# Kernel optimization log

Measured on AMD Instinct MI355X. Metric: run time of the kernel, lower is better.

## Reference

```python
import jax, jax.numpy as jnp
import numpy as np

NUM_HEADS = 16


def setup_inputs() -> dict:
    key = jax.random.key(0)
    ks = jax.random.split(key, 8)
    B, S, H = 2, 2048, 1024
    sd = 1.0 / np.sqrt(H)
    return {
        "x": jax.random.normal(ks[0], (B, S, H), dtype=jnp.float32),
        "mask": jax.random.randint(ks[1], (B, S), 0, 2, dtype=jnp.int32),
        "wq": jax.random.normal(ks[2], (H, H), dtype=jnp.float32) * sd,
        "bq": jnp.zeros((H,), jnp.float32),
        "wk": jax.random.normal(ks[3], (H, H), dtype=jnp.float32) * sd,
        "bk": jnp.zeros((H,), jnp.float32),
        "wv": jax.random.normal(ks[4], (H, H), dtype=jnp.float32) * sd,
        "bv": jnp.zeros((H,), jnp.float32),
        "wo": jax.random.normal(ks[5], (H, H), dtype=jnp.float32) * sd,
        "bo": jnp.zeros((H,), jnp.float32),
        "wg": jax.random.normal(ks[6], (H, H), dtype=jnp.float32) * sd,
        "bg": jnp.zeros((H,), jnp.float32),
    }


def reference(x, mask, wq, bq, wk, bk, wv, bv, wo, bo, wg, bg):
    B, S, H = x.shape
    nh = NUM_HEADS
    hd = H // nh
    scale = hd ** -0.5

    def split_heads(t):  # [B,S,H] -> [B,nh,S,hd]
        return t.reshape(B, S, nh, hd).transpose(0, 2, 1, 3)

    q = split_heads(x @ wq.T + bq)
    k = split_heads(x @ wk.T + bk)
    v = split_heads(x @ wv.T + bv)

    scores = jnp.einsum("bhqd,bhkd->bhqk", q, k) * scale
    # key-padding mask broadcast to [B,1,1,S]
    scores = jnp.where(mask[:, None, None, :] == 0, jnp.float32(-10000.0), scores)
    attn_weights = jax.nn.softmax(scores, axis=-1)  # dropout is identity in eval

    context = jnp.einsum("bhqk,bhkd->bhqd", attn_weights, v)
    context = context.transpose(0, 2, 1, 3).reshape(B, S, H)

    gate_values = jax.nn.sigmoid(context @ wg.T + bg)
    output = (context @ wo.T + bo) * gate_values
    return output, attn_weights
```

## Files before the change

### kernel.cpp

```cpp
#include <hip/hip_runtime.h>
#include <math.h>

#define BB 2
#define SS 2048
#define HH 1024
#define NH 16
#define HD 64
#define LDK 40

typedef __attribute__((ext_vector_type(8))) short short8;
typedef __attribute__((ext_vector_type(4))) float floatx4;

__device__ __forceinline__ unsigned short f2bf(float f) {
    unsigned u = __float_as_uint(f);
    u += 0x7FFF + ((u >> 16) & 1);
    return (unsigned short)(u >> 16);
}
__device__ __forceinline__ float bf2f(unsigned short h) {
    return __uint_as_float((unsigned)h << 16);
}
__device__ __forceinline__ short8 mkshort8(unsigned d0, unsigned d1, unsigned d2, unsigned d3) {
    union { unsigned u[4]; short8 s; } t;
    t.u[0] = d0; t.u[1] = d1; t.u[2] = d2; t.u[3] = d3;
    return t.s;
}

struct SplitJob { const float* src; unsigned short* dh; unsigned short* dl; int n; };
struct SplitJobs { SplitJob j[6]; };

__global__ __launch_bounds__(256) void presplit(SplitJobs jobs)
{
    SplitJob jb = jobs.j[blockIdx.y];
    const int i = (blockIdx.x * 256 + threadIdx.x) * 8;
    if (i >= jb.n) return;
    float4 v0 = *(const float4*)(jb.src + i);
    float4 v1 = *(const float4*)(jb.src + i + 4);
    float f[8] = {v0.x, v0.y, v0.z, v0.w, v1.x, v1.y, v1.z, v1.w};
    union { unsigned short s[8]; uint4 v; } h, l;
#pragma unroll
    for (int j = 0; j < 8; ++j) {
        const unsigned short hs = f2bf(f[j]);
        h.s[j] = hs;
        l.s[j] = f2bf(f[j] - bf2f(hs));
    }
    *(uint4*)(jb.dh + i) = h.v;
    *(uint4*)(jb.dl + i) = l.v;
}

__global__ __launch_bounds__(256) void vtranspose_bf(
    const unsigned short* __restrict__ Vh, const unsigned short* __restrict__ Vl,
    unsigned short* __restrict__ VTh, unsigned short* __restrict__ VTl)
{
    __shared__ __attribute__((aligned(16))) unsigned short t[64][72];
    const int zz = blockIdx.z;
    const int b = zz >> 1;
    const unsigned short* V = (zz & 1) ? Vl : Vh;
    unsigned short* VT = (zz & 1) ? VTl : VTh;
    const int k0 = blockIdx.x * 64;
    const int h = blockIdx.y;
    const int tid = threadIdx.x;
    {
        const int row = tid >> 2, c0 = (tid & 3) * 16;
        const int sw = ((row >> 4) & 3) << 4;
        const unsigned short* g = V + (size_t)(b * SS + k0 + row) * (3 * HH) + h * HD + c0;
        uint4 u0 = *(const uint4*)g;
        uint4 u1 = *(const uint4*)(g + 8);
        *(uint4*)&t[row][c0 ^ sw] = u0;
        *(uint4*)&t[row][(c0 ^ sw) + 8] = u1;
    }
    __syncthreads();
    {
        const int d = tid >> 2, kq = tid & 3;
        const int cs = d ^ (kq << 4);
        union { unsigned short s[16]; uint4 v[2]; } o;
#pragma unroll
        for (int i = 0; i < 16; ++i) o.s[i] = t[kq * 16 + i][cs];
        unsigned short* p = VT + ((size_t)(b * NH + h) * HD + d) * SS + k0 + kq * 16;
        *(uint4*)p = o.v[0];
        *(uint4*)(p + 8) = o.v[1];
    }
}

__global__ __launch_bounds__(256) void attn_fused(
    const unsigned short* __restrict__ QKVh, const unsigned short* __restrict__ QKVl,
    const unsigned short* __restrict__ VTh, const unsigned short* __restrict__ VTl,
    const int* __restrict__ mask,
    float* __restrict__ attn,
    unsigned short* __restrict__ CTXh, unsigned short* __restrict__ CTXl)
{
    __shared__ __attribute__((aligned(16))) unsigned int PS[64 * 64];
    __shared__ float sums[2][64];

    const int tid = threadIdx.x;
    const int wave = tid >> 6, lane = tid & 63;
    const int wm = wave >> 1, wn = wave & 1;
    const int r16 = lane & 15, quad = lane >> 4;

    const int m0 = blockIdx.x * 64;
    const int z  = blockIdx.y;
    const int bz = z >> 4, hz = z & 15;

    short8 fqh[2][2], fql[2][2];
#pragma unroll
    for (int mt = 0; mt < 2; ++mt)
#pragma unroll
        for (int ks = 0; ks < 2; ++ks) {
            const size_t off = (size_t)(bz * SS + m0 + wm * 32 + mt * 16 + r16) * (3 * HH)
                             + hz * HD + ks * 32 + quad * 8;
            fqh[mt][ks] = *(const short8*)(QKVh + off);
            fql[mt][ks] = *(const short8*)(QKVl + off);
        }

    float rsum[2][4];
#pragma unroll
    for (int mt = 0; mt < 2; ++mt)
#pragma unroll
        for (int r = 0; r < 4; ++r) rsum[mt][r] = 0.f;

    for (int nb = 0; nb < 32; ++nb) {
        const int kv0 = nb * 64;
        short8 fkh[2][2], fkl[2][2];
        int mv[2];
#pragma unroll
        for (int nt = 0; nt < 2; ++nt) {
            const int kvr = kv0 + wn * 32 + nt * 16 + r16;
            mv[nt] = mask[bz * SS + kvr];
#pragma unroll
            for (int ks = 0; ks < 2; ++ks) {
                const size_t off = (size_t)(bz * SS + kvr) * (3 * HH) + HH + hz * HD
                                 + ks * 32 + quad * 8;
                fkh[nt][ks] = *(const short8*)(QKVh + off);
                fkl[nt][ks] = *(const short8*)(QKVl + off);
            }
        }
        floatx4 p[2][2];
#pragma unroll
        for (int mt = 0; mt < 2; ++mt)
#pragma unroll
            for (int nt = 0; nt < 2; ++nt) p[mt][nt] = (floatx4){0.f, 0.f, 0.f, 0.f};
#pragma unroll
        for (int mt = 0; mt < 2; ++mt)
#pragma unroll
            for (int nt = 0; nt < 2; ++nt)
#pragma unroll
                for (int ks = 0; ks < 2; ++ks) {
                    p[mt][nt] = __builtin_amdgcn_mfma_f32_16x16x32_bf16(fqh[mt][ks], fkh[nt][ks], p[mt][nt], 0, 0, 0);
                    p[mt][nt] = __builtin_amdgcn_mfma_f32_16x16x32_bf16(fqh[mt][ks], fkl[nt][ks], p[mt][nt], 0, 0, 0);
                    p[mt][nt] = __builtin_amdgcn_mfma_f32_16x16x32_bf16(fql[mt][ks], fkh[nt][ks], p[mt][nt], 0, 0, 0);
                }
#pragma unroll
        for (int mt = 0; mt < 2; ++mt)
#pragma unroll
            for (int nt = 0; nt < 2; ++nt)
#pragma unroll
                for (int r = 0; r < 4; ++r) {
                    const float e = mv[nt] ? __expf(p[mt][nt][r] * 0.125f) : 0.f;
                    rsum[mt][r] += e;
                }
    }
#pragma unroll
    for (int mt = 0; mt < 2; ++mt)
#pragma unroll
        for (int r = 0; r < 4; ++r) {
            float sv = rsum[mt][r];
            sv += __shfl_xor(sv, 1); sv += __shfl_xor(sv, 2);
            sv += __shfl_xor(sv, 4); sv += __shfl_xor(sv, 8);
            if (r16 == 0) sums[wn][wm * 32 + mt * 16 + quad * 4 + r] = sv;
        }
    __syncthreads();
    float inv[2][4];
#pragma unroll
    for (int mt = 0; mt < 2; ++mt)
#pragma unroll
        for (int r = 0; r < 4; ++r) {
            const int row = wm * 32 + mt * 16 + quad * 4 + r;
            inv[mt][r] = 1.0f / (sums[0][row] + sums[1][row]);
        }

    floatx4 accc[2][2];
#pragma unroll
    for (int mt = 0; mt < 2; ++mt)
#pragma unroll
        for (int nt = 0; nt < 2; ++nt) accc[mt][nt] = (floatx4){0.f, 0.f, 0.f, 0.f};

    for (int nb = 0; nb < 32; ++nb) {
        const int kv0 = nb * 64;
        short8 fvh[2][2], fvl[2][2];
#pragma unroll
        for (int nt = 0; nt < 2; ++nt)
#pragma unroll
            for (int kk = 0; kk < 2; ++kk) {
                const size_t off = ((size_t)z * HD + wn * 32 + nt * 16 + r16) * SS
                                 + kv0 + kk * 32 + quad * 8;
                fvh[nt][kk] = *(const short8*)(VTh + off);
                fvl[nt][kk] = *(const short8*)(VTl + off);
            }
        short8 fkh[2][2], fkl[2][2];
        int mv[2];
#pragma unroll
        for (int nt = 0; nt < 2; ++nt) {
            const int kvr = kv0 + wn * 32 + nt * 16 + r16;
            mv[nt] = mask[bz * SS + kvr];
#pragma unroll
            for (int ks = 0; ks < 2; ++ks) {
                const size_t off = (size_t)(bz * SS + kvr) * (3 * HH) + HH + hz * HD
                                 + ks * 32 + quad * 8;
                fkh[nt][ks] = *(const short8*)(QKVh + off);
                fkl[nt][ks] = *(const short8*)(QKVl + off);
            }
        }
        floatx4 p[2][2];
#pragma unroll
        for (int mt = 0; mt < 2; ++mt)
#pragma unroll
            for (int nt = 0; nt < 2; ++nt) p[mt][nt] = (floatx4){0.f, 0.f, 0.f, 0.f};
#pragma unroll
        for (int mt = 0; mt < 2; ++mt)
#pragma unroll
            for (int nt = 0; nt < 2; ++nt)
#pragma unroll
                for (int ks = 0; ks < 2; ++ks) {
                    p[mt][nt] = __builtin_amdgcn_mfma_f32_16x16x32_bf16(fqh[mt][ks], fkh[nt][ks], p[mt][nt], 0, 0, 0);
                    p[mt][nt] = __builtin_amdgcn_mfma_f32_16x16x32_bf16(fqh[mt][ks], fkl[nt][ks], p[mt][nt], 0, 0, 0);
                    p[mt][nt] = __builtin_amdgcn_mfma_f32_16x16x32_bf16(fql[mt][ks], fkh[nt][ks], p[mt][nt], 0, 0, 0);
                }
        __syncthreads();
#pragma unroll
        for (int nt = 0; nt < 2; ++nt) {
            const int kvc = wn * 32 + nt * 16 + r16;
#pragma unroll
            for (int mt = 0; mt < 2; ++mt) {
                const int qb = wm * 32 + mt * 16 + quad * 4;
#pragma unroll
                for (int r = 0; r < 4; ++r) {
                    const float e = mv[nt] ? __expf(p[mt][nt][r] * 0.125f) : 0.f;
                    const float pn = e * inv[mt][r];
                    attn[((size_t)z * SS + m0 + qb + r) * SS + kv0 + kvc] = pn;
                    const unsigned short hv = f2bf(pn);
                    const unsigned short lv = f2bf(pn - bf2f(hv));
                    const int qrow = qb + r;
                    PS[qrow * 64 + (kvc ^ ((qrow & 7) << 2))] =
                        (unsigned)hv | ((unsigned)lv << 16);
                }
            }
        }
        __syncthreads();
#pragma unroll
        for (int mt = 0; mt < 2; ++mt) {
            const int q = wm * 32 + mt * 16 + r16;
            const int sw = (q & 7) << 2;
#pragma unroll
            for (int kk = 0; kk < 2; ++kk) {
                const int kvb = kk * 32 + quad * 8;
                const uint4 a = *(const uint4*)&PS[q * 64 + (kvb ^ sw)];
                const uint4 b = *(const uint4*)&PS[q * 64 + ((kvb + 4) ^ sw)];
                const short8 pah = mkshort8((a.x & 0xffffu) | (a.y << 16),
                                            (a.z & 0xffffu) | (a.w << 16),
                                            (b.x & 0xffffu) | (b.y << 16),
                                            (b.z & 0xffffu) | (b.w << 16));
                const short8 pal = mkshort8((a.x >> 16) | (a.y & 0xffff0000u),
                                            (a.z >> 16) | (a.w & 0xffff0000u),
                                            (b.x >> 16) | (b.y & 0xffff0000u),
                                            (b.z >> 16) | (b.w & 0xffff0000u));
#pragma unroll
                for (int nt = 0; nt < 2; ++nt) {
                    accc[mt][nt] = __builtin_amdgcn_mfma_f32_16x16x32_bf16(pah, fvh[nt][kk], accc[mt][nt], 0, 0, 0);
                    accc[mt][nt] = __builtin_amdgcn_mfma_f32_16x16x32_bf16(pah, fvl[nt][kk], accc[mt][nt], 0, 0, 0);
                    accc[mt][nt] = __builtin_amdgcn_mfma_f32_16x16x32_bf16(pal, fvh[nt][kk], accc[mt][nt], 0, 0, 0);
                }
            }
        }
    }
#pragma unroll
    for (int nt = 0; nt < 2; ++nt) {
        const int dcol = hz * HD + wn * 32 + nt * 16 + r16;
#pragma unroll
        for (int mt = 0; mt < 2; ++mt) {
            const int tok = bz * SS + m0 + wm * 32 + mt * 16 + quad * 4;
#pragma unroll
            for (int r = 0; r < 4; ++r) {
                const float vv = accc[mt][nt][r];
                const unsigned short hv = f2bf(vv);
                const size_t idx = (size_t)(tok + r) * HH + dcol;
                CTXh[idx] = hv;
                CTXl[idx] = f2bf(vv - bf2f(hv));
            }
        }
    }
}

template<int BN, int MODE>
__global__ __launch_bounds__(256) void gemm_bf(
    const unsigned short* __restrict__ Ah, const unsigned short* __restrict__ Al,
    const unsigned short* __restrict__ Bh, const unsigned short* __restrict__ Bl,
    const unsigned short* __restrict__ B2h, const unsigned short* __restrict__ B2l,
    const float* __restrict__ bias, const float* __restrict__ bias2, const float* __restrict__ bias3,
    float* __restrict__ Cf, unsigned short* __restrict__ Ch, unsigned short* __restrict__ Cl,
    int K, int lda, int ldb, int ldc)
{
    constexpr int BM = 128;
    constexpr int MT = 4;
    constexpr int NT = BN / 32;
    constexpr int NSET = (MODE == 3) ? 2 : 1;

    __shared__ __attribute__((aligned(16))) unsigned short AhS[BM * LDK];
    __shared__ __attribute__((aligned(16))) unsigned short AlS[BM * LDK];
    __shared__ __attribute__((aligned(16))) unsigned short BhS[NSET * BN * LDK];
    __shared__ __attribute__((aligned(16))) unsigned short BlS[NSET * BN * LDK];

    const int tid  = threadIdx.x;
    const int lane = tid & 63;
    const int wave = tid >> 6;
    const int wm = wave >> 1, wn = wave & 1;
    const int r16 = lane & 15, quad = lane >> 4;

    const int m0 = blockIdx.y * BM;
    const int n0 = blockIdx.x * BN;

    floatx4 acc[MT][NT][NSET];
#pragma unroll
    for (int mt = 0; mt < MT; ++mt)
#pragma unroll
        for (int nt = 0; nt < NT; ++nt)
#pragma unroll
            for (int s = 0; s < NSET; ++s)
                acc[mt][nt][s] = (floatx4){0.f, 0.f, 0.f, 0.f};

    const int arow = tid >> 1, ac = (tid & 1) * 16;
    const int brow = (BN == 128) ? (tid >> 1) : (tid >> 2);
    const int bc   = (BN == 128) ? ((tid & 1) * 16) : ((tid & 3) * 8);

    const unsigned short* aph = Ah + (size_t)(m0 + arow) * lda + ac;
    const unsigned short* apl = Al + (size_t)(m0 + arow) * lda + ac;
    const unsigned short* bph = Bh + (size_t)(n0 + brow) * ldb + bc;
    const unsigned short* bpl = Bl + (size_t)(n0 + brow) * ldb + bc;
    const unsigned short* b2ph = nullptr;
    const unsigned short* b2pl = nullptr;
    if constexpr (MODE == 3) {
        b2ph = B2h + (size_t)(n0 + brow) * ldb + bc;
        b2pl = B2l + (size_t)(n0 + brow) * ldb + bc;
    }

    for (int kb = 0; kb < K; kb += 32) {
        uint4 avh0 = *(const uint4*)(aph + kb);
        uint4 avh1 = *(const uint4*)(aph + kb + 8);
        uint4 avl0 = *(const uint4*)(apl + kb);
        uint4 avl1 = *(const uint4*)(apl + kb + 8);
        uint4 bvh0 = *(const uint4*)(bph + kb);
        uint4 bvl0 = *(const uint4*)(bpl + kb);
        uint4 bvh1, bvl1, cvh0, cvl0;
        if constexpr (BN == 128) {
            bvh1 = *(const uint4*)(bph + kb + 8);
            bvl1 = *(const uint4*)(bpl + kb + 8);
        }
        if constexpr (MODE == 3) {
            cvh0 = *(const uint4*)(b2ph + kb);
            cvl0 = *(const uint4*)(b2pl + kb);
        }
        __syncthreads();
        *(uint4*)&AhS[arow * LDK + ac]     = avh0;
        *(uint4*)&AhS[arow * LDK + ac + 8] = avh1;
        *(uint4*)&AlS[arow * LDK + ac]     = avl0;
        *(uint4*)&AlS[arow * LDK + ac + 8] = avl1;
        *(uint4*)&BhS[brow * LDK + bc] = bvh0;
        *(uint4*)&BlS[brow * LDK + bc] = bvl0;
        if constexpr (BN == 128) {
            *(uint4*)&BhS[brow * LDK + bc + 8] = bvh1;
            *(uint4*)&BlS[brow * LDK + bc + 8] = bvl1;
        }
        if constexpr (MODE == 3) {
            *(uint4*)&BhS[BN * LDK + brow * LDK + bc] = cvh0;
            *(uint4*)&BlS[BN * LDK + brow * LDK + bc] = cvl0;
        }
        __syncthreads();

        short8 fah[MT], fal[MT], fbh[NSET][NT], fbl[NSET][NT];
#pragma unroll
        for (int mt = 0; mt < MT; ++mt) {
            const int rr = (wm * 64 + mt * 16 + r16) * LDK + quad * 8;
            fah[mt] = *(const short8*)&AhS[rr];
            fal[mt] = *(const short8*)&AlS[rr];
        }
#pragma unroll
        for (int s = 0; s < NSET; ++s)
#pragma unroll
            for (int nt = 0; nt < NT; ++nt) {
                const int rr = s * BN * LDK + (wn * (BN / 2) + nt * 16 + r16) * LDK + quad * 8;
                fbh[s][nt] = *(const short8*)&BhS[rr];
                fbl[s][nt] = *(const short8*)&BlS[rr];
            }
#pragma unroll
        for (int mt = 0; mt < MT; ++mt)
#pragma unroll
            for (int nt = 0; nt < NT; ++nt)
#pragma unroll
                for (int s = 0; s < NSET; ++s) {
                    acc[mt][nt][s] = __builtin_amdgcn_mfma_f32_16x16x32_bf16(fah[mt], fbh[s][nt], acc[mt][nt][s], 0, 0, 0);
                    acc[mt][nt][s] = __builtin_amdgcn_mfma_f32_16x16x32_bf16(fah[mt], fbl[s][nt], acc[mt][nt][s], 0, 0, 0);
                    acc[mt][nt][s] = __builtin_amdgcn_mfma_f32_16x16x32_bf16(fal[mt], fbh[s][nt], acc[mt][nt][s], 0, 0, 0);
                }
    }

    if constexpr (MODE == 0) {
#pragma unroll
        for (int nt = 0; nt < NT; ++nt) {
            const int col = n0 + wn * (BN / 2) + nt * 16 + r16;
            const int seg = col >> 10;
            const float* bp = (seg == 0) ? bias : ((seg == 1) ? bias2 : bias3);
            const float bval = bp[col & (HH - 1)];
#pragma unroll
            for (int mt = 0; mt < MT; ++mt) {
                const int rowb = m0 + wm * 64 + mt * 16 + quad * 4;
#pragma unroll
                for (int r = 0; r < 4; ++r) {
                    const float v = acc[mt][nt][0][r] + bval;
                    const unsigned short hv = f2bf(v);
                    const size_t idx = (size_t)(rowb + r) * ldc + col;
                    Ch[idx] = hv;
                    Cl[idx] = f2bf(v - bf2f(hv));
                }
            }
        }
    }
    if constexpr (MODE == 3) {
#pragma unroll
        for (int nt = 0; nt < NT; ++nt) {
            const int col = n0 + wn * (BN / 2) + nt * 16 + r16;
            const float bov = bias[col], bgv = bias2[col];
#pragma unroll
            for (int mt = 0; mt < MT; ++mt) {
                const int rowb = m0 + wm * 64 + mt * 16 + quad * 4;
#pragma unroll
                for (int r = 0; r < 4; ++r) {
                    const float o = acc[mt][nt][0][r] + bov;
                    const float g = acc[mt][nt][1][r] + bgv;
                    Cf[(size_t)(rowb + r) * ldc + col] = o / (1.f + __expf(-g));
                }
            }
        }
    }
}

extern "C" void kernel_launch(void* const* d_in, const int* in_sizes, int n_in,
                              void* d_out, int out_size, void* d_ws, size_t ws_size,
                              hipStream_t stream)
{
    const float* x    = (const float*)d_in[0];
    const int*   mask = (const int*)d_in[1];
    const float* wq = (const float*)d_in[2];  const float* bq = (const float*)d_in[3];
    const float* wk = (const float*)d_in[4];  const float* bk = (const float*)d_in[5];
    const float* wv = (const float*)d_in[6];  const float* bv = (const float*)d_in[7];
    const float* wo = (const float*)d_in[8];  const float* bo = (const float*)d_in[9];
    const float* wg = (const float*)d_in[10]; const float* bg = (const float*)d_in[11];

    const int M = BB * SS;
    const size_t NTOK = (size_t)M * HH;
    const size_t W1   = (size_t)HH * HH;
    const size_t QKVE = (size_t)M * 3 * HH;

    float* out_main = (float*)d_out;
    float* attn     = (float*)d_out + NTOK;

    unsigned short* p = (unsigned short*)d_ws;
    unsigned short* xh   = p;  p += NTOK;
    unsigned short* xl   = p;  p += NTOK;
    unsigned short* Wqh  = p;  p += 3 * W1;
    unsigned short* Wql  = p;  p += 3 * W1;
    unsigned short* Wgh  = p;  p += 2 * W1;
    unsigned short* Wgl  = p;  p += 2 * W1;
    unsigned short* QKVh = p;  p += QKVE;
    unsigned short* QKVl = p;  p += QKVE;
    unsigned short* VTh  = p;  p += NTOK;
    unsigned short* VTl  = p;  p += NTOK;

    unsigned short* CTXh = xh;
    unsigned short* CTXl = xl;

    SplitJobs jobs;
    jobs.j[0] = SplitJob{x,  xh,           xl,           (int)NTOK};
    jobs.j[1] = SplitJob{wq, Wqh,          Wql,          (int)W1};
    jobs.j[2] = SplitJob{wk, Wqh + W1,     Wql + W1,     (int)W1};
    jobs.j[3] = SplitJob{wv, Wqh + 2 * W1, Wql + 2 * W1, (int)W1};
    jobs.j[4] = SplitJob{wo, Wgh,          Wgl,          (int)W1};
    jobs.j[5] = SplitJob{wg, Wgh + W1,     Wgl + W1,     (int)W1};
    presplit<<<dim3(2048, 6, 1), 256, 0, stream>>>(jobs);

    gemm_bf<128, 0><<<dim3(24, 32, 1), 256, 0, stream>>>(
        xh, xl, Wqh, Wql, nullptr, nullptr,
        bq, bk, bv,
        nullptr, QKVh, QKVl,
        HH, HH, HH, 3 * HH);

    vtranspose_bf<<<dim3(SS / 64, NH, 2 * BB), 256, 0, stream>>>(
        QKVh + 2 * HH, QKVl + 2 * HH, VTh, VTl);

    attn_fused<<<dim3(SS / 64, BB * NH, 1), 256, 0, stream>>>(
        QKVh, QKVl, VTh, VTl, mask, attn, CTXh, CTXl);

    gemm_bf<64, 3><<<dim3(16, 32, 1), 256, 0, stream>>>(
        CTXh, CTXl, Wgh, Wgl, Wgh + W1, Wgl + W1,
        bo, bg, nullptr,
        out_main, nullptr, nullptr,
        HH, HH, HH, HH);

    (void)in_sizes; (void)n_in; (void)out_size; (void)ws_size;
}
```

Baseline: 1.104 ms.

## Stage K tiles into LDS via async global_load_lds and swizzle block-to-XCD mapping

Attention now loads each 64-row K tile (hi and lo bf16 planes) cooperatively into double-buffered, XOR-swizzled shared memory using global_load_lds. The next tile is prefetched while the current one is computed. Previously every wave read K fragments straight from global memory, each wave fetching overlapping data. Block indices in both the attention and GEMM kernels are remapped so that workgroups sharing the same head or tiles land on the same XCD, aiming for better L2 reuse. This adds 32KB of LDS and extra barriers per iteration, which may lower occupancy.

```diff
diff --git a/kernel.cpp b/kernel.cpp
--- a/kernel.cpp
+++ b/kernel.cpp
@@ -10,6 +10,9 @@
 
 typedef __attribute__((ext_vector_type(8))) short short8;
 typedef __attribute__((ext_vector_type(4))) float floatx4;
+
+typedef const __attribute__((address_space(1))) unsigned int* gas1_t;
+typedef __attribute__((address_space(3))) unsigned int* las3_t;
 
 __device__ __forceinline__ unsigned short f2bf(float f) {
     unsigned u = __float_as_uint(f);
@@ -81,6 +84,23 @@
     }
 }
 
+__device__ __forceinline__ void stage_k(
+    unsigned short* KS, const unsigned short* QKVh, const unsigned short* QKVl,
+    int buf, int bz, int hz, int kv0, int tid)
+{
+#pragma unroll
+    for (int i = 0; i < 2; ++i) {
+        const int cid = i * 256 + tid;
+        const int row = cid >> 3;
+        const int cs  = (cid & 7) ^ (row & 7);
+        const size_t goff = (size_t)(bz * SS + kv0 + row) * (3 * HH) + HH + hz * HD + cs * 8;
+        __builtin_amdgcn_global_load_lds((gas1_t)(const void*)(QKVh + goff),
+            (las3_t)(void*)(KS + (buf * 2 + 0) * 4096 + cid * 8), 16, 0, 0);
+        __builtin_amdgcn_global_load_lds((gas1_t)(const void*)(QKVl + goff),
+            (las3_t)(void*)(KS + (buf * 2 + 1) * 4096 + cid * 8), 16, 0, 0);
+    }
+}
+
 __global__ __launch_bounds__(256) void attn_fused(
     const unsigned short* __restrict__ QKVh, const unsigned short* __restrict__ QKVl,
     const unsigned short* __restrict__ VTh, const unsigned short* __restrict__ VTl,
@@ -89,6 +109,7 @@
     unsigned short* __restrict__ CTXh, unsigned short* __restrict__ CTXl)
 {
     __shared__ __attribute__((aligned(16))) unsigned int PS[64 * 64];
+    __shared__ __attribute__((aligned(16))) unsigned short KS[4 * 4096];
     __shared__ float sums[2][64];
 
     const int tid = threadIdx.x;
@@ -96,8 +117,10 @@
     const int wm = wave >> 1, wn = wave & 1;
     const int r16 = lane & 15, quad = lane >> 4;
 
-    const int m0 = blockIdx.x * 64;
-    const int z  = blockIdx.y;
+    const int lin = blockIdx.y * 32 + blockIdx.x;
+    const int swz = (lin & 7) * 128 + (lin >> 3);
+    const int m0 = (swz & 31) * 64;
+    const int z  = swz >> 5;
     const int bz = z >> 4, hz = z & 15;
 
     short8 fqh[2][2], fql[2][2];
@@ -111,26 +134,34 @@
             fql[mt][ks] = *(const short8*)(QKVl + off);
         }
 
+    stage_k(KS, QKVh, QKVl, 0, bz, hz, 0, tid);
+    __syncthreads();
+
     float rsum[2][4];
 #pragma unroll
     for (int mt = 0; mt < 2; ++mt)
 #pragma unroll
         for (int r = 0; r < 4; ++r) rsum[mt][r] = 0.f;
 
+    int cur = 0;
     for (int nb = 0; nb < 32; ++nb) {
         const int kv0 = nb * 64;
+        const int nxt = (nb + 1 < 32) ? (nb + 1) * 64 : 0;
+        stage_k(KS, QKVh, QKVl, cur ^ 1, bz, hz, nxt, tid);
+        int mv[2];
+#pragma unroll
+        for (int nt = 0; nt < 2; ++nt)
+            mv[nt] = mask[bz * SS + kv0 + wn * 32 + nt * 16 + r16];
         short8 fkh[2][2], fkl[2][2];
-        int mv[2];
 #pragma unroll
         for (int nt = 0; nt < 2; ++nt) {
-            const int kvr = kv0 + wn * 32 + nt * 16 + r16;
-            mv[nt] = mask[bz * SS + kvr];
+            const int row = wn * 32 + nt * 16 + r16;
+            const int sx = row & 7;
 #pragma unroll
             for (int ks = 0; ks < 2; ++ks) {
-                const size_t off = (size_t)(bz * SS + kvr) * (3 * HH) + HH + hz * HD
-                                 + ks * 32 + quad * 8;
-                fkh[nt][ks] = *(const short8*)(QKVh + off);
-                fkl[nt][ks] = *(const short8*)(QKVl + off);
+                const int off = row * 64 + ((ks * 4 + quad) ^ sx) * 8;
+                fkh[nt][ks] = *(const short8*)&KS[(cur * 2 + 0) * 4096 + off];
+                fkl[nt][ks] = *(const short8*)&KS[(cur * 2 + 1) * 4096 + off];
             }
         }
         floatx4 p[2][2];
@@ -157,6 +188,8 @@
                     const float e = mv[nt] ? __expf(p[mt][nt][r] * 0.125f) : 0.f;
                     rsum[mt][r] += e;
                 }
+        __syncthreads();
+        cur ^= 1;
     }
 #pragma unroll
     for (int mt = 0; mt < 2; ++mt)
@@ -185,6 +218,7 @@
 
     for (int nb = 0; nb < 32; ++nb) {
         const int kv0 = nb * 64;
+        if (nb + 1 < 32) stage_k(KS, QKVh, QKVl, cur ^ 1, bz, hz, (nb + 1) * 64, tid);
         short8 fvh[2][2], fvl[2][2];
 #pragma unroll
         for (int nt = 0; nt < 2; ++nt)
@@ -195,18 +229,20 @@
                 fvh[nt][kk] = *(const short8*)(VTh + off);
                 fvl[nt][kk] = *(const short8*)(VTl + off);
             }
+        int mv[2];
+#pragma unroll
+        for (int nt = 0; nt < 2; ++nt)
+            mv[nt] = mask[bz * SS + kv0 + wn * 32 + nt * 16 + r16];
         short8 fkh[2][2], fkl[2][2];
-        int mv[2];
 #pragma unroll
         for (int nt = 0; nt < 2; ++nt) {
-            const int kvr = kv0 + wn * 32 + nt * 16 + r16;
-            mv[nt] = mask[bz * SS + kvr];
+            const int row = wn * 32 + nt * 16 + r16;
+            const int sx = row & 7;
 #pragma unroll
             for (int ks = 0; ks < 2; ++ks) {
-                const size_t off = (size_t)(bz * SS + kvr) * (3 * HH) + HH + hz * HD
-                                 + ks * 32 + quad * 8;
-                fkh[nt][ks] = *(const short8*)(QKVh + off);
-                fkl[nt][ks] = *(const short8*)(QKVl + off);
+                const int off = row * 64 + ((ks * 4 + quad) ^ sx) * 8;
+                fkh[nt][ks] = *(const short8*)&KS[(cur * 2 + 0) * 4096 + off];
+                fkl[nt][ks] = *(const short8*)&KS[(cur * 2 + 1) * 4096 + off];
             }
         }
         floatx4 p[2][2];
@@ -270,6 +306,7 @@
                 }
             }
         }
+        cur ^= 1;
     }
 #pragma unroll
     for (int nt = 0; nt < 2; ++nt) {
@@ -314,8 +351,17 @@
     const int wm = wave >> 1, wn = wave & 1;
     const int r16 = lane & 15, quad = lane >> 4;
 
-    const int m0 = blockIdx.y * BM;
-    const int n0 = blockIdx.x * BN;
+    const int gx = gridDim.x;
+    const int nwg = gx * gridDim.y;
+    int bx = blockIdx.x, by = blockIdx.y;
+    if ((nwg & 7) == 0) {
+        const int linid = by * gx + bx;
+        const int q = nwg >> 3;
+        const int s = (linid & 7) * q + (linid >> 3);
+        bx = s % gx; by = s / gx;
+    }
+    const int m0 = by * BM;
+    const int n0 = bx * BN;
 
     floatx4 acc[MT][NT][NSET];
 #pragma unroll
```

Measured after the change: 998.5 us. 9.6% less time.
